# Kernel optimization log

Measured on AMD Instinct MI355X. Metric: run time of the kernel, lower is better.

The kernel has to match this reference:

```python
import jax, jax.numpy as jnp
import numpy as np

T, B, INP, HS, OUT = 1024, 64, 512, 1024, 512


def bump(x):
    # BumpFunction forward: binary gate (straight-through estimator in bwd)
    return (x > 0).astype(x.dtype)


def setup_inputs() -> dict:
    key = jax.random.key(0)
    ks = jax.random.split(key, 12)
    s_in = 1.0 / np.sqrt(INP)
    s_hs = 1.0 / np.sqrt(HS)
    mu_t, sg_t = 0.7, 0.2      # threshold init: |U| * sigma + mu
    mu_d, sg_d = 0.1, 0.7      # decay init
    return {
        "data": jax.random.normal(ks[0], (T, B, INP), jnp.float32),
        # layer 1 (inp -> hs)
        "W1":  jax.random.uniform(ks[1], (HS, INP), jnp.float32, -s_in, s_in),
        "b1":  jnp.zeros((HS,), jnp.float32),
        "Wi1": jax.random.uniform(ks[2], (HS, INP), jnp.float32, -s_in, s_in),
        "bi1": jnp.zeros((HS,), jnp.float32),
        "t1":  jnp.abs(jax.random.uniform(ks[3], (HS,), jnp.float32)) * sg_t + mu_t,
        "dr1": jnp.abs(jax.random.uniform(ks[4], (HS,), jnp.float32)) * sg_d + mu_d,
        # layer 2 (hs -> hs)
        "W2":  jax.random.uniform(ks[5], (HS, HS), jnp.float32, -s_hs, s_hs),
        "b2":  jnp.zeros((HS,), jnp.float32),
        "Wi2": jax.random.uniform(ks[6], (HS, HS), jnp.float32, -s_hs, s_hs),
        "bi2": jnp.zeros((HS,), jnp.float32),
        "t2":  jnp.abs(jax.random.uniform(ks[7], (HS,), jnp.float32)) * sg_t + mu_t,
        "dr2": jnp.abs(jax.random.uniform(ks[8], (HS,), jnp.float32)) * sg_d + mu_d,
        # readout (hs -> out)
        "W3":  jax.random.uniform(ks[9], (OUT, HS), jnp.float32, -s_hs, s_hs),
        "b3":  jnp.zeros((OUT,), jnp.float32),
    }


def reference(data, W1, b1, Wi1, bi1, t1, dr1, W2, b2, Wi2, bi2, t2, dr2, W3, b3):
    # Dropout in eval mode (identity). Only the last timestep's output is returned.
    Bsz = data.shape[1]
    h1_0 = jnp.zeros((Bsz, HS), data.dtype)
    h2_0 = jnp.zeros((Bsz, HS), data.dtype)

    def step(carry, x):
        h1, h2 = carry
        # InhibitAddDecay layer 1: x_a = x_i = x
        a1 = jax.nn.sigmoid(x @ Wi1.T + bi1)            # [B, HS] inhibit activation
        g1 = bump(jax.nn.relu(a1 - t1))                 # binary gate
        h1 = h1 * g1 * dr1 + x @ W1.T + b1              # inhibit, decay, add
        an1 = jnp.tanh(h1)
        # layer 2: x_a = an1, x_i = a1 (inhibit output of layer 1)
        a2 = jax.nn.sigmoid(a1 @ Wi2.T + bi2)
        g2 = bump(jax.nn.relu(a2 - t2))
        h2 = h2 * g2 * dr2 + an1 @ W2.T + b2
        return (h1, h2), None

    (h1_f, h2_f), _ = jax.lax.scan(step, (h1_0, h2_0), data)
    an2 = jnp.tanh(h2_f)
    return an2 @ W3.T + b3                              # [B, OUT]
```

## Files before the change

### kernel.cpp

```cpp
#include <hip/hip_runtime.h>
#include <hip/hip_bf16.h>

#define T_STEPS 1024
#define BATCH   64
#define INP_    512
#define HS_     1024
#define OUT_    512
#define MROWS   (T_STEPS*BATCH)
#define NE      (BATCH*HS_)
#define CH      16
#define CL      (T_STEPS/CH)

typedef __bf16 bf16;
typedef bf16  bf16x8 __attribute__((ext_vector_type(8)));
typedef bf16  bf16x4 __attribute__((ext_vector_type(4)));
typedef bf16  bf16x2 __attribute__((ext_vector_type(2)));
typedef float f32x4  __attribute__((ext_vector_type(4)));

__device__ __forceinline__ void gload_lds16(const bf16* g, bf16* l) {
  __builtin_amdgcn_global_load_lds(
      (const __attribute__((address_space(1))) void*)g,
      (__attribute__((address_space(3))) void*)l,
      16, 0, 0);
}

__device__ __forceinline__ float ftanh(float x) {
  float e = __expf(2.f * x);
  return 1.f - 2.f / (e + 1.f);
}

__global__ void f2b(const float* __restrict__ in, bf16* __restrict__ out, int n4) {
  int stride = gridDim.x * blockDim.x;
  for (int i = blockIdx.x * blockDim.x + threadIdx.x; i < n4; i += stride) {
    float4 v = ((const float4*)in)[i];
    bf16x4 o;
    o[0] = (bf16)v.x; o[1] = (bf16)v.y; o[2] = (bf16)v.z; o[3] = (bf16)v.w;
    ((bf16x4*)out)[i] = o;
  }
}

template<int MODE>
__global__ __launch_bounds__(256, 2)
void gemm_bt(const bf16* __restrict__ A, const bf16* __restrict__ Bw,
             const float* __restrict__ bias, const float* __restrict__ thr,
             bf16* __restrict__ C, unsigned char* __restrict__ Gate,
             int N, int K, int nbn) {
  __shared__ __align__(16) bf16 lds[2][2][128 * 32];
  const int tid  = threadIdx.x;
  const int wave = tid >> 6, lane = tid & 63;
  const int br = blockIdx.x / nbn, bc = blockIdx.x % nbn;
  const int wr = wave >> 1, wc = wave & 1;

  const bf16* Ag = A  + (size_t)br * 128 * K;
  const bf16* Bg = Bw + (size_t)bc * 128 * K;

  f32x4 acc[4][4];
  #pragma unroll
  for (int m = 0; m < 4; ++m)
    #pragma unroll
    for (int n = 0; n < 4; ++n) {
      f32x4 z = {0.f, 0.f, 0.f, 0.f};
      acc[m][n] = z;
    }

  const int nk = K >> 5;
  int cur = 0;

  #pragma unroll
  for (int i = 0; i < 2; ++i) {
    int cg = (i * 4 + wave) * 64;
    int c  = cg + lane;
    int row = c >> 2, kc = c & 3;
    gload_lds16(Ag + (size_t)row * K + kc * 8, &lds[0][0][0] + cg * 8);
    gload_lds16(Bg + (size_t)row * K + kc * 8, &lds[0][1][0] + cg * 8);
  }
  __syncthreads();

  for (int ks = 0; ks < nk; ++ks) {
    if (ks + 1 < nk) {
      const bf16* Agk = Ag + (ks + 1) * 32;
      const bf16* Bgk = Bg + (ks + 1) * 32;
      #pragma unroll
      for (int i = 0; i < 2; ++i) {
        int cg = (i * 4 + wave) * 64;
        int c  = cg + lane;
        int row = c >> 2, kc = c & 3;
        gload_lds16(Agk + (size_t)row * K + kc * 8, &lds[cur ^ 1][0][0] + cg * 8);
        gload_lds16(Bgk + (size_t)row * K + kc * 8, &lds[cur ^ 1][1][0] + cg * 8);
      }
    }
    const bf16* lA = &lds[cur][0][0] + (wr * 64 + (lane & 15)) * 32 + (lane >> 4) * 8;
    const bf16* lB = &lds[cur][1][0] + (wc * 64 + (lane & 15)) * 32 + (lane >> 4) * 8;
    bf16x8 af[4], bfr[4];
    #pragma unroll
    for (int m = 0; m < 4; ++m) af[m]  = *(const bf16x8*)(lA + m * 512);
    #pragma unroll
    for (int n = 0; n < 4; ++n) bfr[n] = *(const bf16x8*)(lB + n * 512);
    #pragma unroll
    for (int m = 0; m < 4; ++m)
      #pragma unroll
      for (int n = 0; n < 4; ++n)
        acc[m][n] = __builtin_amdgcn_mfma_f32_16x16x32_bf16(af[m], bfr[n], acc[m][n], 0, 0, 0);
    __syncthreads();
    cur ^= 1;
  }

  const int rowbase0 = br * 128 + wr * 64 + ((lane >> 4) << 2);
  const int colbase  = bc * 128 + wc * 64 + (lane & 15);
  #pragma unroll
  for (int n = 0; n < 4; ++n) {
    int col = colbase + n * 16;
    float bv = bias[col];
    float tv = 0.f;
    if (MODE >= 1) tv = thr[col];
    #pragma unroll
    for (int m = 0; m < 4; ++m) {
      int row = rowbase0 + m * 16;
      #pragma unroll
      for (int j = 0; j < 4; ++j) {
        float v = acc[m][n][j] + bv;
        size_t off = (size_t)(row + j) * N + col;
        if (MODE == 0) {
          C[off] = (bf16)v;
        } else {
          float a = 1.f / (1.f + __expf(-v));
          if (MODE == 1) { C[off] = (bf16)a; Gate[off] = (a > tv) ? 1 : 0; }
          else           { Gate[off] = (a > tv) ? 1 : 0; }
        }
      }
    }
  }
}

__global__ __launch_bounds__(256)
void scan_p1(const bf16* __restrict__ Z, const unsigned char* __restrict__ G,
             const float* __restrict__ dr, float* __restrict__ Ab,
             float* __restrict__ Bb) {
  int idx = blockIdx.x * 256 + threadIdx.x;
  int c  = idx >> 15;
  int pe = idx & 32767;
  int e  = pe << 1;
  int h  = e & (HS_ - 1);
  float d0 = dr[h], d1 = dr[h + 1];
  float A0 = 1.f, A1 = 1.f, B0 = 0.f, B1 = 0.f;
  size_t base = (size_t)c * CL * NE + e;
  #pragma unroll 8
  for (int t = 0; t < CL; ++t, base += NE) {
    unsigned int zraw = *(const unsigned int*)(Z + base);
    unsigned short graw = *(const unsigned short*)(G + base);
    float z0 = __uint_as_float(zraw << 16);
    float z1 = __uint_as_float(zraw & 0xffff0000u);
    float a0 = (graw & 0x00ff) ? d0 : 0.f;
    float a1 = (graw & 0xff00) ? d1 : 0.f;
    B0 = B0 * a0 + z0;  A0 *= a0;
    B1 = B1 * a1 + z1;  A1 *= a1;
  }
  ((float2*)(Ab + ((size_t)c << 16)))[pe] = make_float2(A0, A1);
  ((float2*)(Bb + ((size_t)c << 16)))[pe] = make_float2(B0, B1);
}

__global__ __launch_bounds__(256)
void scan_p2(const float* __restrict__ Ab, const float* __restrict__ Bb,
             float* __restrict__ Hin) {
  int e = blockIdx.x * 256 + threadIdx.x;
  float h = 0.f;
  #pragma unroll
  for (int c = 0; c < CH; ++c) {
    size_t o = ((size_t)c << 16) + e;
    Hin[o] = h;
    h = Ab[o] * h + Bb[o];
  }
}

__global__ __launch_bounds__(256)
void scan_p2_final(const float* __restrict__ Ab, const float* __restrict__ Bb,
                   float* __restrict__ an2) {
  int e = blockIdx.x * 256 + threadIdx.x;
  float h = 0.f;
  #pragma unroll
  for (int c = 0; c < CH; ++c) {
    size_t o = ((size_t)c << 16) + e;
    h = Ab[o] * h + Bb[o];
  }
  an2[e] = ftanh(h);
}

__global__ __launch_bounds__(256)
void scan_p3(const bf16* __restrict__ Z, const unsigned char* __restrict__ G,
             const float* __restrict__ dr, const float* __restrict__ Hin,
             bf16* __restrict__ AN) {
  int idx = blockIdx.x * 256 + threadIdx.x;
  int c  = idx >> 15;
  int pe = idx & 32767;
  int e  = pe << 1;
  int h  = e & (HS_ - 1);
  float d0 = dr[h], d1 = dr[h + 1];
  float2 hin = ((const float2*)(Hin + ((size_t)c << 16)))[pe];
  float h0 = hin.x, h1 = hin.y;
  size_t base = (size_t)c * CL * NE + e;
  #pragma unroll 4
  for (int t = 0; t < CL; ++t, base += NE) {
    unsigned int zraw = *(const unsigned int*)(Z + base);
    unsigned short graw = *(const unsigned short*)(G + base);
    float z0 = __uint_as_float(zraw << 16);
    float z1 = __uint_as_float(zraw & 0xffff0000u);
    float a0 = (graw & 0x00ff) ? d0 : 0.f;
    float a1 = (graw & 0xff00) ? d1 : 0.f;
    h0 = h0 * a0 + z0;
    h1 = h1 * a1 + z1;
    bf16x2 o;
    o[0] = (bf16)ftanh(h0);
    o[1] = (bf16)ftanh(h1);
    *(bf16x2*)(AN + base) = o;
  }
}

__global__ __launch_bounds__(256)
void readout(const float* __restrict__ an2, const float* __restrict__ W3,
             const float* __restrict__ b3, float* __restrict__ out) {
  int idx = blockIdx.x * 256 + threadIdx.x;
  int b = idx >> 9, o = idx & 511;
  const float4* a = (const float4*)(an2 + (size_t)b * HS_);
  const float4* w = (const float4*)(W3 + (size_t)o * HS_);
  float s = 0.f;
  #pragma unroll 4
  for (int k = 0; k < HS_ / 4; ++k) {
    float4 x = a[k], y = w[k];
    s += x.x * y.x + x.y * y.y + x.z * y.z + x.w * y.w;
  }
  out[idx] = s + b3[o];
}

extern "C" void kernel_launch(void* const* d_in, const int* in_sizes, int n_in,
                              void* d_out, int out_size, void* d_ws, size_t ws_size,
                              hipStream_t stream) {
  const float* data = (const float*)d_in[0];
  const float* W1   = (const float*)d_in[1];
  const float* b1   = (const float*)d_in[2];
  const float* Wi1  = (const float*)d_in[3];
  const float* bi1  = (const float*)d_in[4];
  const float* t1   = (const float*)d_in[5];
  const float* dr1  = (const float*)d_in[6];
  const float* W2   = (const float*)d_in[7];
  const float* b2   = (const float*)d_in[8];
  const float* Wi2  = (const float*)d_in[9];
  const float* bi2  = (const float*)d_in[10];
  const float* t2   = (const float*)d_in[11];
  const float* dr2  = (const float*)d_in[12];
  const float* W3   = (const float*)d_in[13];
  const float* b3   = (const float*)d_in[14];

  char* p = (char*)d_ws;
  bf16* Xbf  = (bf16*)p; p += (size_t)MROWS * INP_ * 2;
  bf16* bufA = (bf16*)p; p += (size_t)MROWS * HS_ * 2;
  bf16* bufB = (bf16*)p; p += (size_t)MROWS * HS_ * 2;
  unsigned char* G1 = (unsigned char*)p; p += (size_t)MROWS * HS_;
  unsigned char* G2 = (unsigned char*)p; p += (size_t)MROWS * HS_;
  bf16* W1b  = (bf16*)p; p += (size_t)HS_ * INP_ * 2;
  bf16* Wi1b = (bf16*)p; p += (size_t)HS_ * INP_ * 2;
  bf16* W2b  = (bf16*)p; p += (size_t)HS_ * HS_ * 2;
  bf16* Wi2b = (bf16*)p; p += (size_t)HS_ * HS_ * 2;
  float* an2 = (float*)p; p += (size_t)NE * 4;
  float* Ab  = (float*)p; p += (size_t)CH * NE * 4;
  float* Bb  = (float*)p; p += (size_t)CH * NE * 4;
  float* Hin = (float*)p; p += (size_t)CH * NE * 4;

  f2b<<<2048, 256, 0, stream>>>(data, Xbf, MROWS * INP_ / 4);
  f2b<<<512,  256, 0, stream>>>(W1,  W1b,  HS_ * INP_ / 4);
  f2b<<<512,  256, 0, stream>>>(Wi1, Wi1b, HS_ * INP_ / 4);
  f2b<<<1024, 256, 0, stream>>>(W2,  W2b,  HS_ * HS_ / 4);
  f2b<<<1024, 256, 0, stream>>>(Wi2, Wi2b, HS_ * HS_ / 4);

  const int nbn = HS_ / 128;
  dim3 gg((MROWS / 128) * nbn);

  gemm_bt<0><<<gg, 256, 0, stream>>>(Xbf, W1b, b1, nullptr, bufA, nullptr, HS_, INP_, nbn);
  gemm_bt<1><<<gg, 256, 0, stream>>>(Xbf, Wi1b, bi1, t1, bufB, G1, HS_, INP_, nbn);
  gemm_bt<2><<<gg, 256, 0, stream>>>(bufB, Wi2b, bi2, t2, nullptr, G2, HS_, HS_, nbn);

  scan_p1<<<CH * NE / 512, 256, 0, stream>>>(bufA, G1, dr1, Ab, Bb);
  scan_p2<<<NE / 256, 256, 0, stream>>>(Ab, Bb, Hin);
  scan_p3<<<CH * NE / 512, 256, 0, stream>>>(bufA, G1, dr1, Hin, bufA);

  gemm_bt<0><<<gg, 256, 0, stream>>>(bufA, W2b, b2, nullptr, bufB, nullptr, HS_, HS_, nbn);

  scan_p1<<<CH * NE / 512, 256, 0, stream>>>(bufB, G2, dr2, Ab, Bb);
  scan_p2_final<<<NE / 256, 256, 0, stream>>>(Ab, Bb, an2);

  readout<<<BATCH * OUT_ / 256, 256, 0, stream>>>(an2, W3, b3, (float*)d_out);
}
```

Before: 1.055 ms.

## Fuse layer-1 GEMMs, add XCD block swizzle, widen scan per-thread width

Concatenates W1 and Wi1 into one weight matrix so layer 1 runs as a single GEMM with N=2048, where each block picks its epilogue (plain bias or sigmoid plus gate) by column half. This reads X once instead of twice and saves a launch. All GEMMs remap block IDs so consecutive tiles land on the same XCD, for better L2 reuse. The scan kernels now handle four elements per thread with wider loads and stores, at the cost of half as many threads.

```diff
diff --git a/kernel.cpp b/kernel.cpp
--- a/kernel.cpp
+++ b/kernel.cpp
@@ -14,7 +14,6 @@
 typedef __bf16 bf16;
 typedef bf16  bf16x8 __attribute__((ext_vector_type(8)));
 typedef bf16  bf16x4 __attribute__((ext_vector_type(4)));
-typedef bf16  bf16x2 __attribute__((ext_vector_type(2)));
 typedef float f32x4  __attribute__((ext_vector_type(4)));
 
 __device__ __forceinline__ void gload_lds16(const bf16* g, bf16* l) {
@@ -27,6 +26,10 @@
 __device__ __forceinline__ float ftanh(float x) {
   float e = __expf(2.f * x);
   return 1.f - 2.f / (e + 1.f);
+}
+
+__device__ __forceinline__ int xcd_swizzle() {
+  return (blockIdx.x & 7) * (gridDim.x >> 3) + (blockIdx.x >> 3);
 }
 
 __global__ void f2b(const float* __restrict__ in, bf16* __restrict__ out, int n4) {
@@ -39,71 +42,67 @@
   }
 }
 
+#define GEMM_BODY(Ag, Bg, K)                                                     \
+  __shared__ __align__(16) bf16 lds[2][2][128 * 32];                             \
+  const int tid  = threadIdx.x;                                                  \
+  const int wave = tid >> 6, lane = tid & 63;                                    \
+  const int wr = wave >> 1, wc = wave & 1;                                       \
+  f32x4 acc[4][4];                                                               \
+  _Pragma("unroll")                                                              \
+  for (int m = 0; m < 4; ++m)                                                    \
+    _Pragma("unroll")                                                            \
+    for (int n = 0; n < 4; ++n) { f32x4 z = {0.f,0.f,0.f,0.f}; acc[m][n] = z; }  \
+  const int nk = (K) >> 5;                                                       \
+  int cur = 0;                                                                   \
+  _Pragma("unroll")                                                              \
+  for (int i = 0; i < 2; ++i) {                                                  \
+    int cg = (i * 4 + wave) * 64;                                                \
+    int c  = cg + lane;                                                          \
+    int row = c >> 2, kc = c & 3;                                                \
+    gload_lds16(Ag + (size_t)row * (K) + kc * 8, &lds[0][0][0] + cg * 8);        \
+    gload_lds16(Bg + (size_t)row * (K) + kc * 8, &lds[0][1][0] + cg * 8);        \
+  }                                                                              \
+  __syncthreads();                                                               \
+  for (int ks = 0; ks < nk; ++ks) {                                              \
+    if (ks + 1 < nk) {                                                           \
+      const bf16* Agk = Ag + (ks + 1) * 32;                                      \
+      const bf16* Bgk = Bg + (ks + 1) * 32;                                      \
+      _Pragma("unroll")                                                          \
+      for (int i = 0; i < 2; ++i) {                                              \
+        int cg = (i * 4 + wave) * 64;                                            \
+        int c  = cg + lane;                                                      \
+        int row = c >> 2, kc = c & 3;                                            \
+        gload_lds16(Agk + (size_t)row * (K) + kc * 8, &lds[cur^1][0][0] + cg*8); \
+        gload_lds16(Bgk + (size_t)row * (K) + kc * 8, &lds[cur^1][1][0] + cg*8); \
+      }                                                                          \
+    }                                                                            \
+    const bf16* lA = &lds[cur][0][0] + (wr * 64 + (lane & 15)) * 32 + (lane >> 4) * 8; \
+    const bf16* lB = &lds[cur][1][0] + (wc * 64 + (lane & 15)) * 32 + (lane >> 4) * 8; \
+    bf16x8 af[4], bfr[4];                                                        \
+    _Pragma("unroll")                                                            \
+    for (int m = 0; m < 4; ++m) af[m]  = *(const bf16x8*)(lA + m * 512);         \
+    _Pragma("unroll")                                                            \
+    for (int n = 0; n < 4; ++n) bfr[n] = *(const bf16x8*)(lB + n * 512);         \
+    _Pragma("unroll")                                                            \
+    for (int m = 0; m < 4; ++m)                                                  \
+      _Pragma("unroll")                                                          \
+      for (int n = 0; n < 4; ++n)                                                \
+        acc[m][n] = __builtin_amdgcn_mfma_f32_16x16x32_bf16(af[m], bfr[n], acc[m][n], 0, 0, 0); \
+    __syncthreads();                                                             \
+    cur ^= 1;                                                                    \
+  }
+
 template<int MODE>
 __global__ __launch_bounds__(256, 2)
 void gemm_bt(const bf16* __restrict__ A, const bf16* __restrict__ Bw,
              const float* __restrict__ bias, const float* __restrict__ thr,
              bf16* __restrict__ C, unsigned char* __restrict__ Gate,
              int N, int K, int nbn) {
-  __shared__ __align__(16) bf16 lds[2][2][128 * 32];
-  const int tid  = threadIdx.x;
-  const int wave = tid >> 6, lane = tid & 63;
-  const int br = blockIdx.x / nbn, bc = blockIdx.x % nbn;
-  const int wr = wave >> 1, wc = wave & 1;
-
+  const int bid = xcd_swizzle();
+  const int br = bid / nbn, bc = bid % nbn;
   const bf16* Ag = A  + (size_t)br * 128 * K;
   const bf16* Bg = Bw + (size_t)bc * 128 * K;
-
-  f32x4 acc[4][4];
-  #pragma unroll
-  for (int m = 0; m < 4; ++m)
-    #pragma unroll
-    for (int n = 0; n < 4; ++n) {
-      f32x4 z = {0.f, 0.f, 0.f, 0.f};
-      acc[m][n] = z;
-    }
-
-  const int nk = K >> 5;
-  int cur = 0;
-
-  #pragma unroll
-  for (int i = 0; i < 2; ++i) {
-    int cg = (i * 4 + wave) * 64;
-    int c  = cg + lane;
-    int row = c >> 2, kc = c & 3;
-    gload_lds16(Ag + (size_t)row * K + kc * 8, &lds[0][0][0] + cg * 8);
-    gload_lds16(Bg + (size_t)row * K + kc * 8, &lds[0][1][0] + cg * 8);
-  }
-  __syncthreads();
-
-  for (int ks = 0; ks < nk; ++ks) {
-    if (ks + 1 < nk) {
-      const bf16* Agk = Ag + (ks + 1) * 32;
-      const bf16* Bgk = Bg + (ks + 1) * 32;
-      #pragma unroll
-      for (int i = 0; i < 2; ++i) {
-        int cg = (i * 4 + wave) * 64;
-        int c  = cg + lane;
-        int row = c >> 2, kc = c & 3;
-        gload_lds16(Agk + (size_t)row * K + kc * 8, &lds[cur ^ 1][0][0] + cg * 8);
-        gload_lds16(Bgk + (size_t)row * K + kc * 8, &lds[cur ^ 1][1][0] + cg * 8);
-      }
-    }
-    const bf16* lA = &lds[cur][0][0] + (wr * 64 + (lane & 15)) * 32 + (lane >> 4) * 8;
-    const bf16* lB = &lds[cur][1][0] + (wc * 64 + (lane & 15)) * 32 + (lane >> 4) * 8;
-    bf16x8 af[4], bfr[4];
-    #pragma unroll
-    for (int m = 0; m < 4; ++m) af[m]  = *(const bf16x8*)(lA + m * 512);
-    #pragma unroll
-    for (int n = 0; n < 4; ++n) bfr[n] = *(const bf16x8*)(lB + n * 512);
-    #pragma unroll
-    for (int m = 0; m < 4; ++m)
-      #pragma unroll
-      for (int n = 0; n < 4; ++n)
-        acc[m][n] = __builtin_amdgcn_mfma_f32_16x16x32_bf16(af[m], bfr[n], acc[m][n], 0, 0, 0);
-    __syncthreads();
-    cur ^= 1;
-  }
+  GEMM_BODY(Ag, Bg, K)
 
   const int rowbase0 = br * 128 + wr * 64 + ((lane >> 4) << 2);
   const int colbase  = bc * 128 + wc * 64 + (lane & 15);
@@ -111,8 +110,7 @@
   for (int n = 0; n < 4; ++n) {
     int col = colbase + n * 16;
     float bv = bias[col];
-    float tv = 0.f;
-    if (MODE >= 1) tv = thr[col];
+    float tv = (MODE == 2) ? thr[col] : 0.f;
     #pragma unroll
     for (int m = 0; m < 4; ++m) {
       int row = rowbase0 + m * 16;
@@ -124,8 +122,48 @@
           C[off] = (bf16)v;
         } else {
           float a = 1.f / (1.f + __expf(-v));
-          if (MODE == 1) { C[off] = (bf16)a; Gate[off] = (a > tv) ? 1 : 0; }
-          else           { Gate[off] = (a > tv) ? 1 : 0; }
+          Gate[off] = (a > tv) ? 1 : 0;
+        }
+      }
+    }
+  }
+}
+
+__global__ __launch_bounds__(256, 2)
+void gemm_l1(const bf16* __restrict__ A, const bf16* __restrict__ Wf,
+             const float* __restrict__ b1, const float* __restrict__ bi1,
+             const float* __restrict__ t1,
+             bf16* __restrict__ C0, bf16* __restrict__ C1,
+             unsigned char* __restrict__ G1) {
+  const int nbn = 16, K = INP_;
+  const int bid = xcd_swizzle();
+  const int br = bid / nbn, bc = bid % nbn;
+  const bf16* Ag = A  + (size_t)br * 128 * K;
+  const bf16* Bg = Wf + (size_t)bc * 128 * K;
+  GEMM_BODY(Ag, Bg, K)
+
+  const int rowbase0 = br * 128 + wr * 64 + ((lane >> 4) << 2);
+  const int colbase  = bc * 128 + wc * 64 + (lane & 15);
+  const bool inh = (bc >= 8);
+  #pragma unroll
+  for (int n = 0; n < 4; ++n) {
+    int col = colbase + n * 16;
+    int lc  = col & (HS_ - 1);
+    float bv = inh ? bi1[lc] : b1[lc];
+    float tv = inh ? t1[lc] : 0.f;
+    #pragma unroll
+    for (int m = 0; m < 4; ++m) {
+      int row = rowbase0 + m * 16;
+      #pragma unroll
+      for (int j = 0; j < 4; ++j) {
+        float v = acc[m][n][j] + bv;
+        size_t off = (size_t)(row + j) * HS_ + lc;
+        if (!inh) {
+          C0[off] = (bf16)v;
+        } else {
+          float a = 1.f / (1.f + __expf(-v));
+          C1[off] = (bf16)a;
+          G1[off] = (a > tv) ? 1 : 0;
         }
       }
     }
@@ -137,26 +175,32 @@
              const float* __restrict__ dr, float* __restrict__ Ab,
              float* __restrict__ Bb) {
   int idx = blockIdx.x * 256 + threadIdx.x;
-  int c  = idx >> 15;
-  int pe = idx & 32767;
-  int e  = pe << 1;
+  int c  = idx >> 14;
+  int q  = idx & 16383;
+  int e  = q << 2;
   int h  = e & (HS_ - 1);
-  float d0 = dr[h], d1 = dr[h + 1];
-  float A0 = 1.f, A1 = 1.f, B0 = 0.f, B1 = 0.f;
+  float d0 = dr[h], d1 = dr[h+1], d2 = dr[h+2], d3 = dr[h+3];
+  float A0=1.f,A1=1.f,A2=1.f,A3=1.f, B0=0.f,B1=0.f,B2=0.f,B3=0.f;
   size_t base = (size_t)c * CL * NE + e;
   #pragma unroll 8
   for (int t = 0; t < CL; ++t, base += NE) {
-    unsigned int zraw = *(const unsigned int*)(Z + base);
-    unsigned short graw = *(const unsigned short*)(G + base);
-    float z0 = __uint_as_float(zraw << 16);
-    float z1 = __uint_as_float(zraw & 0xffff0000u);
-    float a0 = (graw & 0x00ff) ? d0 : 0.f;
-    float a1 = (graw & 0xff00) ? d1 : 0.f;
-    B0 = B0 * a0 + z0;  A0 *= a0;
-    B1 = B1 * a1 + z1;  A1 *= a1;
-  }
-  ((float2*)(Ab + ((size_t)c << 16)))[pe] = make_float2(A0, A1);
-  ((float2*)(Bb + ((size_t)c << 16)))[pe] = make_float2(B0, B1);
+    uint2 zr = *(const uint2*)(Z + base);
+    unsigned int gr = *(const unsigned int*)(G + base);
+    float z0 = __uint_as_float(zr.x << 16);
+    float z1 = __uint_as_float(zr.x & 0xffff0000u);
+    float z2 = __uint_as_float(zr.y << 16);
+    float z3 = __uint_as_float(zr.y & 0xffff0000u);
+    float a0 = (gr & 0x000000ffu) ? d0 : 0.f;
+    float a1 = (gr & 0x0000ff00u) ? d1 : 0.f;
+    float a2 = (gr & 0x00ff0000u) ? d2 : 0.f;
+    float a3 = (gr & 0xff000000u) ? d3 : 0.f;
+    B0 = B0*a0 + z0;  A0 *= a0;
+    B1 = B1*a1 + z1;  A1 *= a1;
+    B2 = B2*a2 + z2;  A2 *= a2;
+    B3 = B3*a3 + z3;  A3 *= a3;
+  }
+  ((float4*)(Ab + ((size_t)c << 16)))[q] = make_float4(A0,A1,A2,A3);
+  ((float4*)(Bb + ((size_t)c << 16)))[q] = make_float4(B0,B1,B2,B3);
 }
 
 __global__ __launch_bounds__(256)
@@ -190,28 +234,32 @@
              const float* __restrict__ dr, const float* __restrict__ Hin,
              bf16* __restrict__ AN) {
   int idx = blockIdx.x * 256 + threadIdx.x;
-  int c  = idx >> 15;
-  int pe = idx & 32767;
-  int e  = pe << 1;
+  int c  = idx >> 14;
+  int q  = idx & 16383;
+  int e  = q << 2;
   int h  = e & (HS_ - 1);
-  float d0 = dr[h], d1 = dr[h + 1];
-  float2 hin = ((const float2*)(Hin + ((size_t)c << 16)))[pe];
-  float h0 = hin.x, h1 = hin.y;
+  float d0 = dr[h], d1 = dr[h+1], d2 = dr[h+2], d3 = dr[h+3];
+  float4 hin = ((const float4*)(Hin + ((size_t)c << 16)))[q];
+  float h0 = hin.x, h1 = hin.y, h2 = hin.z, h3 = hin.w;
   size_t base = (size_t)c * CL * NE + e;
   #pragma unroll 4
   for (int t = 0; t < CL; ++t, base += NE) {
-    unsigned int zraw = *(const unsigned int*)(Z + base);
-    unsigned short graw = *(const unsigned short*)(G + base);
-    float z0 = __uint_as_float(zraw << 16);
-    float z1 = __uint_as_float(zraw & 0xffff0000u);
-    float a0 = (graw & 0x00ff) ? d0 : 0.f;
-    float a1 = (graw & 0xff00) ? d1 : 0.f;
-    h0 = h0 * a0 + z0;
-    h1 = h1 * a1 + z1;
-    bf16x2 o;
+    uint2 zr = *(const uint2*)(Z + base);
+    unsigned int gr = *(const unsigned int*)(G + base);
+    float z0 = __uint_as_float(zr.x << 16);
+    float z1 = __uint_as_float(zr.x & 0xffff0000u);
+    float z2 = __uint_as_float(zr.y << 16);
+    float z3 = __uint_as_float(zr.y & 0xffff0000u);
+    h0 = h0 * ((gr & 0x000000ffu) ? d0 : 0.f) + z0;
+    h1 = h1 * ((gr & 0x0000ff00u) ? d1 : 0.f) + z1;
+    h2 = h2 * ((gr & 0x00ff0000u) ? d2 : 0.f) + z2;
+    h3 = h3 * ((gr & 0xff000000u) ? d3 : 0.f) + z3;
+    bf16x4 o;
     o[0] = (bf16)ftanh(h0);
     o[1] = (bf16)ftanh(h1);
-    *(bf16x2*)(AN + base) = o;
+    o[2] = (bf16)ftanh(h2);
+    o[3] = (bf16)ftanh(h3);
+    *(bf16x4*)(AN + base) = o;
   }
 }
 
@@ -256,8 +304,7 @@
   bf16* bufB = (bf16*)p; p += (size_t)MROWS * HS_ * 2;
   unsigned char* G1 = (unsigned char*)p; p += (size_t)MROWS * HS_;
   unsigned char* G2 = (unsigned char*)p; p += (size_t)MROWS * HS_;
-  bf16* W1b  = (bf16*)p; p += (size_t)HS_ * INP_ * 2;
-  bf16* Wi1b = (bf16*)p; p += (size_t)HS_ * INP_ * 2;
+  bf16* Wf   = (bf16*)p; p += (size_t)2 * HS_ * INP_ * 2;
   bf16* W2b  = (bf16*)p; p += (size_t)HS_ * HS_ * 2;
   bf16* Wi2b = (bf16*)p; p += (size_t)HS_ * HS_ * 2;
   float* an2 = (float*)p; p += (size_t)NE * 4;
@@ -266,25 +313,25 @@
   float* Hin = (float*)p; p += (size_t)CH * NE * 4;
 
   f2b<<<2048, 256, 0, stream>>>(data, Xbf, MROWS * INP_ / 4);
-  f2b<<<512,  256, 0, stream>>>(W1,  W1b,  HS_ * INP_ / 4);
-  f2b<<<512,  256, 0, stream>>>(Wi1, Wi1b, HS_ * INP_ / 4);
+  f2b<<<512,  256, 0, stream>>>(W1,  Wf,              HS_ * INP_ / 4);
+  f2b<<<512,  256, 0, stream>>>(Wi1, Wf + HS_ * INP_, HS_ * INP_ / 4);
   f2b<<<1024, 256, 0, stream>>>(W2,  W2b,  HS_ * HS_ / 4);
   f2b<<<1024, 256, 0, stream>>>(Wi2, Wi2b, HS_ * HS_ / 4);
 
+  gemm_l1<<<dim3((MROWS / 128) * 16), 256, 0, stream>>>(Xbf, Wf, b1, bi1, t1, bufA, bufB, G1);
+
   const int nbn = HS_ / 128;
   dim3 gg((MROWS / 128) * nbn);
 
-  gemm_bt<0><<<gg, 256, 0, stream>>>(Xbf, W1b, b1, nullptr, bufA, nullptr, HS_, INP_, nbn);
-  gemm_bt<1><<<gg, 256, 0, stream>>>(Xbf, Wi1b, bi1, t1, bufB, G1, HS_, INP_, nbn);
   gemm_bt<2><<<gg, 256, 0, stream>>>(bufB, Wi2b, bi2, t2, nullptr, G2, HS_, HS_, nbn);
 
-  scan_p1<<<CH * NE / 512, 256, 0, stream>>>(bufA, G1, dr1, Ab, Bb);
+  scan_p1<<<CH * NE / 1024, 256, 0, stream>>>(bufA, G1, dr1, Ab, Bb);
   scan_p2<<<NE / 256, 256, 0, stream>>>(Ab, Bb, Hin);
-  scan_p3<<<CH * NE / 512, 256, 0, stream>>>(bufA, G1, dr1, Hin, bufA);
+  scan_p3<<<CH * NE / 1024, 256, 0, stream>>>(bufA, G1, dr1, Hin, bufA);
 
   gemm_bt<0><<<gg, 256, 0, stream>>>(bufA, W2b, b2, nullptr, bufB, nullptr, HS_, HS_, nbn);
 
-  scan_p1<<<CH * NE / 512, 256, 0, stream>>>(bufB, G2, dr2, Ab, Bb);
+  scan_p1<<<CH * NE / 1024, 256, 0, stream>>>(bufB, G2, dr2, Ab, Bb);
   scan_p2_final<<<NE / 256, 256, 0, stream>>>(Ab, Bb, an2);
 
   readout<<<BATCH * OUT_ / 256, 256, 0, stream>>>(an2, W3, b3, (float*)d_out);
```

Result: faster. 1.033 ms (-2.1%).
